# Performance work log

Hardware: AMD Instinct MI355X
Metric: run time of the kernel (lower is better)

## Reference

```python
import jax, jax.numpy as jnp
import numpy as np
from jax.ops import segment_sum, segment_max

N, D, B = 1536, 32, 8            # nodes, candidate out-degree per node, sequential batch steps
OBS, HID, HEADS, C = 33, 64, 4, 8  # obs_dim, GRU hidden, attn heads, out_dim//heads
E = N * D


def setup_inputs() -> dict:
    key = jax.random.key(0)
    ks = jax.random.split(key, 16)
    g = lambda i, shape, s=0.1: jax.random.normal(ks[i], shape, jnp.float32) * s
    src = jnp.repeat(jnp.arange(N), D)                    # uniform degree -> scatter_topk = row top-k
    dst = jax.random.randint(ks[0], (E,), 0, N)
    return dict(
        H_t=jax.random.normal(ks[1], (B, N, OBS), jnp.float32),
        src=src, dst=dst, k=4,
        W_e1=g(2, (OBS, 32)), b_e1=jnp.zeros(32), W_e2=g(3, (32, 32)), b_e2=jnp.zeros(32),
        ln_g=jnp.ones(32), ln_b=jnp.zeros(32),
        W_ih=g(4, (3 * HID, 32)), W_hh=g(5, (3 * HID, HID)),
        b_ih=jnp.zeros(3 * HID), b_hh=jnp.zeros(3 * HID),
        W_s1=g(6, (2 * HID, 64)), b_s1=jnp.zeros(64), W_s2=g(7, (64, 1)), b_s2=jnp.zeros(1),
        W_gat=g(8, (HID, HEADS * C)), att_src=g(9, (HEADS, C)), att_dst=g(10, (HEADS, C)),
        b_gat=jnp.zeros(HEADS * C),
    )


def _layernorm(x, g, b, eps=1e-5):
    mu = x.mean(-1, keepdims=True)
    var = ((x - mu) ** 2).mean(-1, keepdims=True)
    return (x - mu) * jax.lax.rsqrt(var + eps) * g + b


def _forward(H_t, src, dst, k, W_e1, b_e1, W_e2, b_e2, ln_g, ln_b,
             W_ih, W_hh, b_ih, b_hh, W_s1, b_s1, W_s2, b_s2,
             W_gat, att_src, att_dst, b_gat):
    # ObsEmbedding: Linear-ReLU-Linear-ReLU-LayerNorm, applied to all (B,N) at once
    x = jax.nn.relu(H_t @ W_e1 + b_e1)
    x = jax.nn.relu(x @ W_e2 + b_e2)
    H_emb = _layernorm(x, ln_g, ln_b)              # (B,N,32)

    def step(h, e_t):
        # --- NodeMemory: shared GRUCell, h carried across batch steps ---
        gi = e_t @ W_ih.T + b_ih                   # (N,3H)
        gh = h @ W_hh.T + b_hh
        i_r, i_z, i_n = jnp.split(gi, 3, -1)
        h_r, h_z, h_n = jnp.split(gh, 3, -1)
        r = jax.nn.sigmoid(i_r + h_r)
        z = jax.nn.sigmoid(i_z + h_z)
        n = jnp.tanh(i_n + r * h_n)
        h_new = (1.0 - z) * n + z * h              # (N,HID)

        # --- EdgeScorer: sigmoid MLP score per candidate edge, keep top-k per source ---
        feat = jnp.concatenate([h_new[src], h_new[dst]], -1)        # (E,2*HID)
        score = jax.nn.sigmoid(
            (jax.nn.relu(feat @ W_s1 + b_s1) @ W_s2 + b_s2)[:, 0])  # (E,)
        s2 = score.reshape(N, D)
        top_idx = jax.lax.top_k(s2, k)[1]                           # (N,k)
        keep = (jnp.zeros((N, D), bool)
                .at[jnp.arange(N)[:, None], top_idx].set(True)).reshape(-1)  # (E,)
        w = jnp.where(keep, score, 0.0)                             # soft edge weights

        # --- GATConv (add_self_loops=False), pruned edges masked out of the softmax ---
        xh = (h_new @ W_gat).reshape(N, HEADS, C)
        a_s = (xh * att_src).sum(-1)               # (N,HEADS)
        a_d = (xh * att_dst).sum(-1)
        logit = jax.nn.leaky_relu(a_s[src] + a_d[dst], 0.2)         # (E,HEADS)
        logit = jnp.where(keep[:, None], logit, -1e30)
        m = segment_max(logit, dst, num_segments=N)                 # softmax grouped by target
        ex = jnp.where(keep[:, None], jnp.exp(logit - m[dst]), 0.0)
        ssum = segment_sum(ex, dst, num_segments=N)
        alpha = ex / jnp.clip(ssum[dst], 1e-16)                     # (E,HEADS)

        msg = alpha[:, :, None] * xh[src] * w[:, None, None]        # edge_weight scales messages
        out = segment_sum(msg, dst, num_segments=N).reshape(N, HEADS * C) + b_gat

        # --- densify attention: scatter-accumulate then row-normalize ---
        A = jnp.zeros((HEADS, N, N), alpha.dtype).at[:, src, dst].add(alpha.T)
        A = A / jnp.clip(A.sum(-1, keepdims=True), 1e-9)
        return h_new, (out, A)

    h0 = jnp.zeros((N, HID), H_t.dtype)
    _, (outs, attns) = jax.lax.scan(step, h0, H_emb)
    return outs, attns                              # (B,N,32), (B,HEADS,N,N)


def reference(H_t, src, dst, k, W_e1, b_e1, W_e2, b_e2, ln_g, ln_b,
              W_ih, W_hh, b_ih, b_hh, W_s1, b_s1, W_s2, b_s2,
              W_gat, att_src, att_dst, b_gat):
    return _forward(H_t, src, dst, k, W_e1, b_e1, W_e2, b_e2, ln_g, ln_b,
                    W_ih, W_hh, b_ih, b_hh, W_s1, b_s1, W_s2, b_s2,
                    W_gat, att_src, att_dst, b_gat)
```

## Files before the change

### kernel.cpp

```cpp
#include <hip/hip_runtime.h>
#include <math.h>

#define NN   1536
#define DG   32
#define BB   8
#define OBSD 33
#define HID  64
#define NHEAD 4
#define EE   (NN*DG)

__device__ __forceinline__ float sigm(float x){ return 1.0f/(1.0f+expf(-x)); }

__global__ void __launch_bounds__(256) k_embgi(
                      const float* __restrict__ Ht,
                      const float* __restrict__ We1, const float* __restrict__ be1,
                      const float* __restrict__ We2, const float* __restrict__ be2,
                      const float* __restrict__ lng, const float* __restrict__ lnb,
                      const float* __restrict__ Wih, const float* __restrict__ bih,
                      float* __restrict__ GI){
    __shared__ float lwih[192*33];
    int tid = threadIdx.x;
    for(int i=tid;i<192*32;i+=256){ int r=i>>5, c=i&31; lwih[r*33+c]=Wih[i]; }
    __syncthreads();
    int lane = tid & 63;
    int j32 = lane & 31;
    int bn = blockIdx.x*4 + (tid>>6);
    const float* hrow = Ht + (size_t)bn*OBSD;
    float x1 = be1[j32];
    for(int o=0;o<OBSD;o++) x1 += hrow[o]*We1[o*32+j32];
    x1 = fmaxf(x1,0.f);
    float x2 = be2[j32];
    for(int i=0;i<32;i++){
        float xi = __shfl(x1, (lane & 32) | i, 64);
        x2 += xi * We2[i*32+j32];
    }
    x2 = fmaxf(x2,0.f);
    float mu = x2;
    for(int m=16;m>=1;m>>=1) mu += __shfl_xor(mu, m, 32);
    mu *= (1.0f/32.0f);
    float d = x2-mu; float var = d*d;
    for(int m=16;m>=1;m>>=1) var += __shfl_xor(var, m, 32);
    var *= (1.0f/32.0f);
    float xln = d*rsqrtf(var+1e-5f)*lng[j32]+lnb[j32];
    int j = lane;
    float gr=bih[j], gz=bih[64+j], gn=bih[128+j];
    for(int kk=0;kk<32;kk++){
        float ek = __shfl(xln, kk, 64);
        gr += ek*lwih[j*33+kk];
        gz += ek*lwih[(64+j)*33+kk];
        gn += ek*lwih[(128+j)*33+kk];
    }
    float* g = GI + (size_t)bn*192;
    g[j]=gr; g[64+j]=gz; g[128+j]=gn;
}

__global__ void k_count(const int* __restrict__ dst, int* __restrict__ cursor){
    int e = blockIdx.x*256+threadIdx.x;
    if(e<EE) atomicAdd(&cursor[dst[e]],1);
}
__global__ void k_scan(int* __restrict__ cnt, int* __restrict__ indptr){
    __shared__ int part[256];
    int t = threadIdx.x;
    int local[6]; int s=0;
    for(int i=0;i<6;i++){ local[i]=cnt[t*6+i]; s+=local[i]; }
    part[t]=s; __syncthreads();
    if(t==0){ int acc=0; for(int i=0;i<256;i++){ int v=part[i]; part[i]=acc; acc+=v; } }
    __syncthreads();
    int pre = part[t];
    for(int i=0;i<6;i++){ int idx=t*6+i; indptr[idx]=pre; cnt[idx]=pre; pre+=local[i]; }
    if(t==255) indptr[NN]=EE;
}
__global__ void k_fill(const int* __restrict__ dst, int* __restrict__ cursor, int* __restrict__ eids){
    int e = blockIdx.x*256+threadIdx.x;
    if(e<EE){ int p = atomicAdd(&cursor[dst[e]],1); eids[p]=e; }
}

__global__ void __launch_bounds__(384) k_gru_all(const float* __restrict__ GI,
                       const float* __restrict__ Whh, const float* __restrict__ bhh,
                       float* __restrict__ Hall){
    __shared__ float lw[192*65];
    int tid = threadIdx.x;
    for(int i=tid;i<192*64;i+=384){ int r=i>>6, c=i&63; lw[r*65+c]=Whh[i]; }
    __syncthreads();
    int node = blockIdx.x*6 + (tid>>6);
    int j = tid&63;
    float b_r=bhh[j], b_z=bhh[64+j], b_n=bhh[128+j];
    const float* lwr = lw + j*65;
    const float* lwz = lw + (64+j)*65;
    const float* lwn = lw + (128+j)*65;
    float hold = 0.f;
    for(int t=0;t<BB;t++){
        float hr=b_r, hz=b_z, hn=b_n;
        for(int kk=0;kk<64;kk++){
            float hk = __shfl(hold,kk);
            hr += hk*lwr[kk];
            hz += hk*lwz[kk];
            hn += hk*lwn[kk];
        }
        const float* g = GI + ((size_t)t*NN+node)*192;
        float r  = sigm(g[j]     + hr);
        float z  = sigm(g[64+j]  + hz);
        float nn_= tanhf(g[128+j] + r*hn);
        hold = (1.f-z)*nn_ + z*hold;
        Hall[((size_t)t*NN+node)*64 + j] = hold;
    }
}

__global__ void __launch_bounds__(256) k_post(const float* __restrict__ Hall,
                       const float* __restrict__ Ws1, const float* __restrict__ Wgat,
                       const float* __restrict__ atts, const float* __restrict__ attd,
                       float* __restrict__ P, float* __restrict__ Q,
                       float* __restrict__ xh, float* __restrict__ as_, float* __restrict__ ad_){
    __shared__ float ws1l[128*64];
    __shared__ float wgl[64*32];
    int tid = threadIdx.x;
    for(int i=tid;i<128*64;i+=256) ws1l[i]=Ws1[i];
    for(int i=tid;i<64*32;i+=256)  wgl[i]=Wgat[i];
    __syncthreads();
    int bn = blockIdx.x*4 + (tid>>6);
    int j = tid&63;
    float hv = Hall[(size_t)bn*64+j];
    float p=0.f,q=0.f,xv=0.f;
    for(int kk=0;kk<64;kk++){
        float hk=__shfl(hv,kk);
        p += hk*ws1l[kk*64+j];
        q += hk*ws1l[(64+kk)*64+j];
        if(j<32) xv += hk*wgl[kk*32+j];
    }
    P[(size_t)bn*64+j]=p; Q[(size_t)bn*64+j]=q;
    if(j<32){
        xh[(size_t)bn*32+j]=xv;
        float asv = xv*atts[j];
        float adv = xv*attd[j];
        for(int m=1;m<8;m<<=1){ asv += __shfl_xor(asv,m); adv += __shfl_xor(adv,m); }
        if((j&7)==0){ as_[(size_t)bn*4+(j>>3)]=asv; ad_[(size_t)bn*4+(j>>3)]=adv; }
    }
}

__global__ void k_edge(const float* __restrict__ P, const float* __restrict__ Q,
                       const float* __restrict__ bs1, const float* __restrict__ Ws2,
                       const float* __restrict__ bs2, const int* __restrict__ dst,
                       const int* __restrict__ kptr, float* __restrict__ wbuf){
    int lane = threadIdx.x;
    int t = blockIdx.y;
    int row = blockIdx.x*2 + (lane>>5);
    int d = lane & 31;
    int e = row*DG + d;
    int de = dst[e];
    const float4* Pr = (const float4*)(P + ((size_t)t*NN+row)*64);
    const float4* Qr = (const float4*)(Q + ((size_t)t*NN+de)*64);
    const float4* B1 = (const float4*)bs1;
    const float4* W2 = (const float4*)Ws2;
    float acc = 0.f;
    #pragma unroll
    for(int jj=0;jj<16;jj++){
        float4 pv=Pr[jj], qv=Qr[jj], bv=B1[jj], wv=W2[jj];
        acc += fmaxf(pv.x+qv.x+bv.x,0.f)*wv.x;
        acc += fmaxf(pv.y+qv.y+bv.y,0.f)*wv.y;
        acc += fmaxf(pv.z+qv.z+bv.z,0.f)*wv.z;
        acc += fmaxf(pv.w+qv.w+bv.w,0.f)*wv.w;
    }
    float score = sigm(acc + bs2[0]);
    int kk = kptr[0]; if(kk>32) kk=32; if(kk<0) kk=0;
    bool sel=false;
    for(int it=0; it<kk; it++){
        float v = sel ? -INFINITY : score;
        int idx = d;
        for(int m=16;m>=1;m>>=1){
            float ov = __shfl_xor(v,m,32);
            int   oi = __shfl_xor(idx,m,32);
            if(ov>v || (ov==v && oi<idx)){ v=ov; idx=oi; }
        }
        if(idx==d) sel=true;
    }
    wbuf[(size_t)t*EE + e] = sel ? score : 0.f;
}

__global__ void __launch_bounds__(256) k_soft(const int* __restrict__ indptr, const int* __restrict__ eids,
                       const int* __restrict__ src,
                       const float* __restrict__ as_, const float* __restrict__ ad_,
                       const float* __restrict__ wbuf, const float* __restrict__ xhb,
                       const float* __restrict__ bgat,
                       float* __restrict__ alphab, float* __restrict__ outp){
    int n = blockIdx.x;
    int t = blockIdx.y;
    int h = threadIdx.x>>6;
    int lane = threadIdx.x&63;
    const float* w     = wbuf  + (size_t)t*EE;
    const float* asb   = as_   + (size_t)t*NN*4;
    const float* xhbt  = xhb   + (size_t)t*NN*32;
    float*       alpha = alphab+ (size_t)t*EE*4;
    int beg = indptr[n], end = indptr[n+1];
    float adv = ad_[((size_t)t*NN+n)*4+h];
    float m = -INFINITY;
    for(int i=beg+lane;i<end;i+=64){
        int e = eids[i];
        if(w[e]>0.f){
            float lg = asb[src[e]*4+h]+adv;
            lg = lg>0.f ? lg : 0.2f*lg;
            m = fmaxf(m,lg);
        }
    }
    for(int mm=32;mm>=1;mm>>=1) m = fmaxf(m,__shfl_xor(m,mm));
    float ssum=0.f;
    for(int i=beg+lane;i<end;i+=64){
        int e = eids[i];
        float ex = 0.f;
        if(w[e]>0.f){
            float lg = asb[src[e]*4+h]+adv;
            lg = lg>0.f ? lg : 0.2f*lg;
            ex = expf(lg-m);
        }
        alpha[e*4+h]=ex;
        ssum += ex;
    }
    for(int mm=32;mm>=1;mm>>=1) ssum += __shfl_xor(ssum,mm);
    float inv = 1.0f/fmaxf(ssum,1e-16f);
    float acc[8];
    #pragma unroll
    for(int c=0;c<8;c++) acc[c]=0.f;
    for(int i=beg+lane;i<end;i+=64){
        int e = eids[i];
        float a = alpha[e*4+h]*inv;
        alpha[e*4+h]=a;
        if(a>0.f){
            float aw = a*w[e];
            const float* xr = xhbt + src[e]*32 + h*8;
            #pragma unroll
            for(int c=0;c<8;c++) acc[c] += aw*xr[c];
        }
    }
    for(int mm=32;mm>=1;mm>>=1){
        #pragma unroll
        for(int c=0;c<8;c++) acc[c] += __shfl_xor(acc[c],mm);
    }
    if(lane==0){
        float* o = outp + ((size_t)t*NN+n)*32 + h*8;
        #pragma unroll
        for(int c=0;c<8;c++) o[c] = acc[c] + bgat[h*8+c];
    }
}

__global__ void __launch_bounds__(256) k_scatter(const float* __restrict__ alphab,
                       const int* __restrict__ dst, float* __restrict__ attn){
    __shared__ float rowbuf[NHEAD][NN];
    __shared__ float rs[NHEAD];
    __shared__ float rsf[NHEAD];
    int n = blockIdx.x;
    int t = blockIdx.y;
    const float* alpha = alphab + (size_t)t*EE*4;
    int tid = threadIdx.x;
    for(int i=tid;i<NHEAD*NN;i+=256) ((float*)rowbuf)[i]=0.f;
    if(tid<NHEAD) rs[tid]=0.f;
    __syncthreads();
    float a=0.f; int de=0; int h=0;
    if(tid<128){
        int d = tid>>2; h = tid&3;
        int e = n*DG+d;
        a = alpha[e*4+h];
        de = dst[e];
        if(a>0.f) atomicAdd(&rs[h], a);
    }
    __syncthreads();
    if(tid<NHEAD) rsf[tid] = 1.0f/fmaxf(rs[tid],1e-9f);
    __syncthreads();
    if(tid<128 && a>0.f) atomicAdd(&rowbuf[h][de], a*rsf[h]);
    __syncthreads();
    size_t tb = (size_t)t*NHEAD*NN*NN;
    for(int i=tid;i<NHEAD*(NN/4);i+=256){
        int hh = i/(NN/4); int c4 = i%(NN/4);
        float4 v = ((const float4*)rowbuf[hh])[c4];
        ((float4*)(attn + tb + (size_t)hh*NN*NN + (size_t)n*NN))[c4] = v;
    }
}

extern "C" void kernel_launch(void* const* d_in, const int* in_sizes, int n_in,
                              void* d_out, int out_size, void* d_ws, size_t ws_size,
                              hipStream_t stream) {
    const float* Ht   = (const float*)d_in[0];
    const int*   src  = (const int*)  d_in[1];
    const int*   dst  = (const int*)  d_in[2];
    const int*   kptr = (const int*)  d_in[3];
    const float* We1  = (const float*)d_in[4];
    const float* be1  = (const float*)d_in[5];
    const float* We2  = (const float*)d_in[6];
    const float* be2  = (const float*)d_in[7];
    const float* lng  = (const float*)d_in[8];
    const float* lnb  = (const float*)d_in[9];
    const float* Wih  = (const float*)d_in[10];
    const float* Whh  = (const float*)d_in[11];
    const float* bih  = (const float*)d_in[12];
    const float* bhh  = (const float*)d_in[13];
    const float* Ws1  = (const float*)d_in[14];
    const float* bs1  = (const float*)d_in[15];
    const float* Ws2  = (const float*)d_in[16];
    const float* bs2  = (const float*)d_in[17];
    const float* Wgat = (const float*)d_in[18];
    const float* atts = (const float*)d_in[19];
    const float* attd = (const float*)d_in[20];
    const float* bgat = (const float*)d_in[21];

    float* outp = (float*)d_out;
    float* attn = outp + (size_t)BB*NN*32;

    float* ws    = (float*)d_ws;
    float* GI    = ws;
    float* Hall  = ws + 2359296;
    float* P     = ws + 3145728;
    float* Q     = ws + 3932160;
    float* xh    = ws + 4718592;
    float* as_   = ws + 5111808;
    float* ad_   = ws + 5160960;
    float* wbuf  = ws + 5210112;
    float* alpha = ws + 5603328;
    int*   ibase = (int*)(ws + 7176192);
    int*   cursor= ibase;
    int*   indptr= ibase + 2048;
    int*   eids  = ibase + 4096;

    hipMemsetAsync(cursor, 0, (size_t)NN*sizeof(int), stream);

    k_embgi<<<BB*NN/4, 256, 0, stream>>>(Ht, We1, be1, We2, be2, lng, lnb, Wih, bih, GI);
    k_count<<<EE/256, 256, 0, stream>>>(dst, cursor);
    k_scan<<<1, 256, 0, stream>>>(cursor, indptr);
    k_fill<<<EE/256, 256, 0, stream>>>(dst, cursor, eids);
    k_gru_all<<<NN/6, 384, 0, stream>>>(GI, Whh, bhh, Hall);
    k_post<<<BB*NN/4, 256, 0, stream>>>(Hall, Ws1, Wgat, atts, attd, P, Q, xh, as_, ad_);
    {
        dim3 g(NN/2, BB);
        k_edge<<<g, 64, 0, stream>>>(P, Q, bs1, Ws2, bs2, dst, kptr, wbuf);
    }
    {
        dim3 g(NN, BB);
        k_soft<<<g, 256, 0, stream>>>(indptr, eids, src, as_, ad_, wbuf, xh, bgat, alpha, outp);
        k_scatter<<<g, 256, 0, stream>>>(alpha, dst, attn);
    }
}
```

Measured before the change: 520.8 us.

## Process all heads per wavefront in softmax kernel and use readlane broadcasts

Restructures the GAT softmax/aggregation kernel so each wavefront handles one destination node across all four heads. It loads attention scores and features as float4 and keeps the first 128 edges in registers between passes, instead of rereading them. Lane broadcasts in the dense matvec kernels switch from shuffles to readlane, and shared-memory zeroing uses vector stores. The cost is higher register pressure from the 32-element accumulator and its cross-lane reductions.

```diff
diff --git a/kernel.cpp b/kernel.cpp
--- a/kernel.cpp
+++ b/kernel.cpp
@@ -10,6 +10,9 @@
 #define EE   (NN*DG)
 
 __device__ __forceinline__ float sigm(float x){ return 1.0f/(1.0f+expf(-x)); }
+__device__ __forceinline__ float rl(float v, int l){
+    return __int_as_float(__builtin_amdgcn_readlane(__float_as_int(v), l));
+}
 
 __global__ void __launch_bounds__(256) k_embgi(
                       const float* __restrict__ Ht,
@@ -31,7 +34,7 @@
     x1 = fmaxf(x1,0.f);
     float x2 = be2[j32];
     for(int i=0;i<32;i++){
-        float xi = __shfl(x1, (lane & 32) | i, 64);
+        float xi = rl(x1, i);
         x2 += xi * We2[i*32+j32];
     }
     x2 = fmaxf(x2,0.f);
@@ -45,7 +48,7 @@
     int j = lane;
     float gr=bih[j], gz=bih[64+j], gn=bih[128+j];
     for(int kk=0;kk<32;kk++){
-        float ek = __shfl(xln, kk, 64);
+        float ek = rl(xln, kk);
         gr += ek*lwih[j*33+kk];
         gz += ek*lwih[(64+j)*33+kk];
         gn += ek*lwih[(128+j)*33+kk];
@@ -92,7 +95,7 @@
     for(int t=0;t<BB;t++){
         float hr=b_r, hz=b_z, hn=b_n;
         for(int kk=0;kk<64;kk++){
-            float hk = __shfl(hold,kk);
+            float hk = rl(hold,kk);
             hr += hk*lwr[kk];
             hz += hk*lwz[kk];
             hn += hk*lwn[kk];
@@ -122,7 +125,7 @@
     float hv = Hall[(size_t)bn*64+j];
     float p=0.f,q=0.f,xv=0.f;
     for(int kk=0;kk<64;kk++){
-        float hk=__shfl(hv,kk);
+        float hk=rl(hv,kk);
         p += hk*ws1l[kk*64+j];
         q += hk*ws1l[(64+kk)*64+j];
         if(j<32) xv += hk*wgl[kk*32+j];
@@ -182,62 +185,152 @@
                        const float* __restrict__ wbuf, const float* __restrict__ xhb,
                        const float* __restrict__ bgat,
                        float* __restrict__ alphab, float* __restrict__ outp){
-    int n = blockIdx.x;
     int t = blockIdx.y;
-    int h = threadIdx.x>>6;
-    int lane = threadIdx.x&63;
-    const float* w     = wbuf  + (size_t)t*EE;
-    const float* asb   = as_   + (size_t)t*NN*4;
-    const float* xhbt  = xhb   + (size_t)t*NN*32;
-    float*       alpha = alphab+ (size_t)t*EE*4;
+    int n = blockIdx.x*4 + (threadIdx.x>>6);
+    int lane = threadIdx.x & 63;
+    const float*  w    = wbuf + (size_t)t*EE;
+    const float4* as4  = (const float4*)(as_ + (size_t)t*NN*4);
+    const float4* ad4v = (const float4*)(ad_ + (size_t)t*NN*4);
+    const float*  xhbt = xhb + (size_t)t*NN*32;
+    float4* alpha      = (float4*)(alphab + (size_t)t*EE*4);
     int beg = indptr[n], end = indptr[n+1];
-    float adv = ad_[((size_t)t*NN+n)*4+h];
-    float m = -INFINITY;
-    for(int i=beg+lane;i<end;i+=64){
-        int e = eids[i];
-        if(w[e]>0.f){
-            float lg = asb[src[e]*4+h]+adv;
-            lg = lg>0.f ? lg : 0.2f*lg;
-            m = fmaxf(m,lg);
-        }
-    }
-    for(int mm=32;mm>=1;mm>>=1) m = fmaxf(m,__shfl_xor(m,mm));
-    float ssum=0.f;
-    for(int i=beg+lane;i<end;i+=64){
-        int e = eids[i];
-        float ex = 0.f;
-        if(w[e]>0.f){
-            float lg = asb[src[e]*4+h]+adv;
-            lg = lg>0.f ? lg : 0.2f*lg;
-            ex = expf(lg-m);
-        }
-        alpha[e*4+h]=ex;
-        ssum += ex;
-    }
-    for(int mm=32;mm>=1;mm>>=1) ssum += __shfl_xor(ssum,mm);
-    float inv = 1.0f/fmaxf(ssum,1e-16f);
-    float acc[8];
-    #pragma unroll
-    for(int c=0;c<8;c++) acc[c]=0.f;
-    for(int i=beg+lane;i<end;i+=64){
-        int e = eids[i];
-        float a = alpha[e*4+h]*inv;
-        alpha[e*4+h]=a;
-        if(a>0.f){
-            float aw = a*w[e];
-            const float* xr = xhbt + src[e]*32 + h*8;
+    float4 adq = ad4v[n];
+    float adv[4] = {adq.x, adq.y, adq.z, adq.w};
+
+    int   i0 = beg + lane, i1 = beg + 64 + lane;
+    int   e0 = 0, e1 = 0, s0 = 0, s1 = 0;
+    float w0 = 0.f, w1 = 0.f;
+    float av0[4]={0.f,0.f,0.f,0.f}, av1[4]={0.f,0.f,0.f,0.f};
+    if(i0 < end){
+        e0 = eids[i0]; w0 = w[e0];
+        if(w0>0.f){ s0 = src[e0]; float4 qv = as4[s0]; av0[0]=qv.x;av0[1]=qv.y;av0[2]=qv.z;av0[3]=qv.w; }
+    }
+    if(i1 < end){
+        e1 = eids[i1]; w1 = w[e1];
+        if(w1>0.f){ s1 = src[e1]; float4 qv = as4[s1]; av1[0]=qv.x;av1[1]=qv.y;av1[2]=qv.z;av1[3]=qv.w; }
+    }
+    float lg0[4], lg1[4], m[4];
+    #pragma unroll
+    for(int h=0;h<4;h++){
+        float l0 = av0[h]+adv[h]; l0 = l0>0.f ? l0 : 0.2f*l0;
+        float l1 = av1[h]+adv[h]; l1 = l1>0.f ? l1 : 0.2f*l1;
+        lg0[h] = (w0>0.f) ? l0 : -INFINITY;
+        lg1[h] = (w1>0.f) ? l1 : -INFINITY;
+        m[h] = fmaxf(lg0[h], lg1[h]);
+    }
+    bool tail = (end - beg) > 128;
+    if(tail){
+        for(int i=beg+128+lane; i<end; i+=64){
+            int e=eids[i]; float wv=w[e];
+            if(wv>0.f){
+                float4 qv = as4[src[e]];
+                float qa[4]={qv.x,qv.y,qv.z,qv.w};
+                #pragma unroll
+                for(int h=0;h<4;h++){ float l=qa[h]+adv[h]; l=l>0.f?l:0.2f*l; m[h]=fmaxf(m[h],l); }
+            }
+        }
+    }
+    #pragma unroll
+    for(int mm=32;mm>=1;mm>>=1){
+        #pragma unroll
+        for(int h=0;h<4;h++) m[h] = fmaxf(m[h], __shfl_xor(m[h], mm));
+    }
+    float ex0[4], ex1[4], ss[4];
+    #pragma unroll
+    for(int h=0;h<4;h++){
+        ex0[h] = (w0>0.f) ? expf(lg0[h]-m[h]) : 0.f;
+        ex1[h] = (w1>0.f) ? expf(lg1[h]-m[h]) : 0.f;
+        ss[h]  = ex0[h]+ex1[h];
+    }
+    if(tail){
+        for(int i=beg+128+lane; i<end; i+=64){
+            int e=eids[i]; float wv=w[e];
+            float exq[4]={0.f,0.f,0.f,0.f};
+            if(wv>0.f){
+                float4 qv = as4[src[e]];
+                float qa[4]={qv.x,qv.y,qv.z,qv.w};
+                #pragma unroll
+                for(int h=0;h<4;h++){ float l=qa[h]+adv[h]; l=l>0.f?l:0.2f*l; exq[h]=expf(l-m[h]); ss[h]+=exq[h]; }
+            }
+            alpha[e] = make_float4(exq[0],exq[1],exq[2],exq[3]);
+        }
+    }
+    #pragma unroll
+    for(int mm=32;mm>=1;mm>>=1){
+        #pragma unroll
+        for(int h=0;h<4;h++) ss[h] += __shfl_xor(ss[h], mm);
+    }
+    float inv[4];
+    #pragma unroll
+    for(int h=0;h<4;h++) inv[h] = 1.0f/fmaxf(ss[h],1e-16f);
+
+    float acc[32];
+    #pragma unroll
+    for(int c=0;c<32;c++) acc[c]=0.f;
+
+    if(i0 < end){
+        float a0[4];
+        #pragma unroll
+        for(int h=0;h<4;h++) a0[h]=ex0[h]*inv[h];
+        alpha[e0] = make_float4(a0[0],a0[1],a0[2],a0[3]);
+        if(w0>0.f){
+            const float4* xr4 = (const float4*)(xhbt + (size_t)s0*32);
             #pragma unroll
-            for(int c=0;c<8;c++) acc[c] += aw*xr[c];
-        }
-    }
+            for(int h=0;h<4;h++){
+                float aw = a0[h]*w0;
+                float4 xa = xr4[h*2], xb = xr4[h*2+1];
+                acc[h*8+0]+=aw*xa.x; acc[h*8+1]+=aw*xa.y; acc[h*8+2]+=aw*xa.z; acc[h*8+3]+=aw*xa.w;
+                acc[h*8+4]+=aw*xb.x; acc[h*8+5]+=aw*xb.y; acc[h*8+6]+=aw*xb.z; acc[h*8+7]+=aw*xb.w;
+            }
+        }
+    }
+    if(i1 < end){
+        float a1[4];
+        #pragma unroll
+        for(int h=0;h<4;h++) a1[h]=ex1[h]*inv[h];
+        alpha[e1] = make_float4(a1[0],a1[1],a1[2],a1[3]);
+        if(w1>0.f){
+            const float4* xr4 = (const float4*)(xhbt + (size_t)s1*32);
+            #pragma unroll
+            for(int h=0;h<4;h++){
+                float aw = a1[h]*w1;
+                float4 xa = xr4[h*2], xb = xr4[h*2+1];
+                acc[h*8+0]+=aw*xa.x; acc[h*8+1]+=aw*xa.y; acc[h*8+2]+=aw*xa.z; acc[h*8+3]+=aw*xa.w;
+                acc[h*8+4]+=aw*xb.x; acc[h*8+5]+=aw*xb.y; acc[h*8+6]+=aw*xb.z; acc[h*8+7]+=aw*xb.w;
+            }
+        }
+    }
+    if(tail){
+        for(int i=beg+128+lane; i<end; i+=64){
+            int e=eids[i]; float wv=w[e];
+            float4 qv = alpha[e];
+            float a[4]={qv.x*inv[0], qv.y*inv[1], qv.z*inv[2], qv.w*inv[3]};
+            alpha[e] = make_float4(a[0],a[1],a[2],a[3]);
+            if(wv>0.f){
+                const float4* xr4 = (const float4*)(xhbt + (size_t)src[e]*32);
+                #pragma unroll
+                for(int h=0;h<4;h++){
+                    float aw = a[h]*wv;
+                    float4 xa = xr4[h*2], xb = xr4[h*2+1];
+                    acc[h*8+0]+=aw*xa.x; acc[h*8+1]+=aw*xa.y; acc[h*8+2]+=aw*xa.z; acc[h*8+3]+=aw*xa.w;
+                    acc[h*8+4]+=aw*xb.x; acc[h*8+5]+=aw*xb.y; acc[h*8+6]+=aw*xb.z; acc[h*8+7]+=aw*xb.w;
+                }
+            }
+        }
+    }
+    #pragma unroll
     for(int mm=32;mm>=1;mm>>=1){
         #pragma unroll
-        for(int c=0;c<8;c++) acc[c] += __shfl_xor(acc[c],mm);
+        for(int c=0;c<32;c++) acc[c] += __shfl_xor(acc[c], mm);
     }
     if(lane==0){
-        float* o = outp + ((size_t)t*NN+n)*32 + h*8;
-        #pragma unroll
-        for(int c=0;c<8;c++) o[c] = acc[c] + bgat[h*8+c];
+        float4* o = (float4*)(outp + ((size_t)t*NN+n)*32);
+        const float4* bg4 = (const float4*)bgat;
+        #pragma unroll
+        for(int q8=0;q8<8;q8++){
+            float4 b = bg4[q8];
+            o[q8] = make_float4(acc[q8*4]+b.x, acc[q8*4+1]+b.y, acc[q8*4+2]+b.z, acc[q8*4+3]+b.w);
+        }
     }
 }
 
@@ -250,7 +343,7 @@
     int t = blockIdx.y;
     const float* alpha = alphab + (size_t)t*EE*4;
     int tid = threadIdx.x;
-    for(int i=tid;i<NHEAD*NN;i+=256) ((float*)rowbuf)[i]=0.f;
+    for(int i=tid;i<NHEAD*(NN/4);i+=256) ((float4*)rowbuf)[i]=make_float4(0.f,0.f,0.f,0.f);
     if(tid<NHEAD) rs[tid]=0.f;
     __syncthreads();
     float a=0.f; int de=0; int h=0;
@@ -331,8 +424,9 @@
         k_edge<<<g, 64, 0, stream>>>(P, Q, bs1, Ws2, bs2, dst, kptr, wbuf);
     }
     {
+        dim3 gs(NN/4, BB);
+        k_soft<<<gs, 256, 0, stream>>>(indptr, eids, src, as_, ad_, wbuf, xh, bgat, alpha, outp);
         dim3 g(NN, BB);
-        k_soft<<<g, 256, 0, stream>>>(indptr, eids, src, as_, ad_, wbuf, xh, bgat, alpha, outp);
         k_scatter<<<g, 256, 0, stream>>>(alpha, dst, attn);
     }
 }
```

New measurement: 490.0 us. 1.06x faster.
